# Kernel tuning notes

Measured on AMD Instinct MI355X. Metric: run time of the kernel, lower is better.

## Reference

```python
import jax, jax.numpy as jnp
import numpy as np

D_MODEL = 1024
N_HEADS = 4
KEY_DIM = 1024   # expand_k=1.0
VALUE_DIM = 2048 # expand_v=2.0
DK = KEY_DIM // N_HEADS    # 256
DV = VALUE_DIM // N_HEADS  # 512
LOW_RANK = 16
GATE_NORM = 16.0
EPS = 1e-5


def setup_inputs() -> dict:
    key = jax.random.key(0)
    ks = jax.random.split(key, 10)
    B, L = 2, 2048
    gain = 2.0 ** (-2.5)

    def xavier(k, shape, g=gain):
        fan_in, fan_out = shape[0], shape[1]
        a = g * np.sqrt(6.0 / (fan_in + fan_out))
        return jax.random.uniform(k, shape, jnp.float32, -a, a)

    return {
        "x": jax.random.normal(ks[0], (B, L, D_MODEL), jnp.float32),
        "Wq": xavier(ks[1], (D_MODEL, KEY_DIM)),
        "Wk": xavier(ks[2], (D_MODEL, KEY_DIM)),
        "Wv": xavier(ks[3], (D_MODEL, VALUE_DIM)),
        "Wg": xavier(ks[4], (D_MODEL, VALUE_DIM)),
        "gk_w1": xavier(ks[5], (D_MODEL, LOW_RANK)),
        "gk_w2": xavier(ks[6], (LOW_RANK, KEY_DIM)),
        "gk_b2": jnp.zeros((KEY_DIM,), jnp.float32),
        "g_norm_w": jnp.ones((DV,), jnp.float32),
        "Wo": xavier(ks[7], (VALUE_DIM, D_MODEL)),
    }


def _gla_scan(q, k, v, gk):
    # q,k: [B,H,L,Dk]; v: [B,H,L,Dv]; gk: [B,H,L,Dk] (log decay)
    # recurrence: S_t = diag(exp(gk_t)) S_{t-1} + k_t v_t^T ; o_t = q_t S_t
    B, H, L, dk = q.shape
    dv = v.shape[-1]
    # time-major for scan
    qs = jnp.moveaxis(q, 2, 0)
    ks_ = jnp.moveaxis(k, 2, 0)
    vs = jnp.moveaxis(v, 2, 0)
    gs = jnp.moveaxis(gk, 2, 0)

    def step(S, inp):
        q_t, k_t, v_t, g_t = inp  # [B,H,Dk], [B,H,Dk], [B,H,Dv], [B,H,Dk]
        S = S * jnp.exp(g_t)[..., None] + k_t[..., None] * v_t[..., None, :]
        o_t = jnp.einsum('bhk,bhkv->bhv', q_t, S)
        return S, o_t

    S0 = jnp.zeros((B, H, dk, dv), q.dtype)
    _, os = jax.lax.scan(step, S0, (qs, ks_, vs, gs))
    return jnp.moveaxis(os, 0, 2)  # [B,H,L,Dv]


def reference(x, Wq, Wk, Wv, Wg, gk_w1, gk_w2, gk_b2, g_norm_w, Wo):
    B, L, _ = x.shape
    scale = DK ** -0.5

    def heads(t, d):
        return t.reshape(B, L, N_HEADS, d).transpose(0, 2, 1, 3)  # b h l d

    q = heads(x @ Wq, DK) * scale
    k = heads(x @ Wk, DK)
    v = heads(x @ Wv, DV)
    gk = heads(jax.nn.log_sigmoid((x @ gk_w1) @ gk_w2 + gk_b2) / GATE_NORM, DK)

    o = _gla_scan(q, k, v, gk)                 # [B,H,L,Dv]
    o = o.transpose(0, 2, 1, 3)                # [B,L,H,Dv]

    g = (x @ Wg).reshape(B, L, N_HEADS, DV)
    # FusedRMSNormSwishGate: RMSNorm(o) * silu(g)
    rms = o * jax.lax.rsqrt(jnp.mean(o * o, axis=-1, keepdims=True) + EPS)
    o = (rms * g_norm_w) * (g * jax.nn.sigmoid(g))
    o = o.reshape(B, L, VALUE_DIM)
    return o @ Wo
```

## Files before the change

kernel.cpp:

```cpp
#include <hip/hip_runtime.h>
#include <hip/hip_bf16.h>
#include <math.h>

#define NHEADS 4
#define DKH 256
#define DVH 512
#define SEQL 2048
#define NB 2
#define NTOK (NB*SEQL)
#define DM 1024
#define KDT 1024
#define VDT 2048
#define CHUNK 128
#define NCH (SEQL/CHUNK)

typedef unsigned short u16;
typedef unsigned int   u32;
typedef unsigned long long u64;
typedef __attribute__((ext_vector_type(8))) short bf16x8;
typedef __attribute__((ext_vector_type(4))) float f32x4;

__device__ inline u16 f2bf(float f) {
  __hip_bfloat16 h = __float2bfloat16(f);
  return *reinterpret_cast<u16*>(&h);
}
__device__ inline float bf2f(u16 u) {
  u32 x = ((u32)u) << 16;
  return __uint_as_float(x);
}

__device__ __forceinline__ void gload16(const u16* g, u16* l) {
  __builtin_amdgcn_global_load_lds(
      (const __attribute__((address_space(1))) u32*)g,
      (__attribute__((address_space(3))) u32*)l,
      16, 0, 0);
}

__global__ __launch_bounds__(256)
void f2bf_kernel(const float* __restrict__ in, u16* __restrict__ out, int n)
{
  const int i = (blockIdx.x * 256 + threadIdx.x) * 8;
  if (i >= n) return;
  const float4 x0 = *(const float4*)&in[i];
  const float4 x1 = *(const float4*)&in[i + 4];
  int4 p;
  p.x = f2bf(x0.x) | ((u32)f2bf(x0.y) << 16);
  p.y = f2bf(x0.z) | ((u32)f2bf(x0.w) << 16);
  p.z = f2bf(x1.x) | ((u32)f2bf(x1.y) << 16);
  p.w = f2bf(x1.z) | ((u32)f2bf(x1.w) << 16);
  *(int4*)&out[i] = p;
}

__global__ __launch_bounds__(256)
void transpose_f2bf(const float* __restrict__ W, u16* __restrict__ Wt, int K, int N)
{
  __shared__ float Ts[64][69];
  const int n0 = blockIdx.x * 64, k0 = blockIdx.y * 64;
  const int tx = threadIdx.x & 15, ty = threadIdx.x >> 4;
  #pragma unroll
  for (int r = 0; r < 4; ++r) {
    const int k = ty + r * 16;
    const float4 w4 = *(const float4*)&W[(size_t)(k0 + k) * N + n0 + tx * 4];
    Ts[tx*4 + 0][k] = w4.x;
    Ts[tx*4 + 1][k] = w4.y;
    Ts[tx*4 + 2][k] = w4.z;
    Ts[tx*4 + 3][k] = w4.w;
  }
  __syncthreads();
  #pragma unroll
  for (int r = 0; r < 4; ++r) {
    const int n = ty + r * 16;
    u64 pk = (u64)f2bf(Ts[n][tx*4 + 0]) | ((u64)f2bf(Ts[n][tx*4 + 1]) << 16)
           | ((u64)f2bf(Ts[n][tx*4 + 2]) << 32) | ((u64)f2bf(Ts[n][tx*4 + 3]) << 48);
    *(u64*)&Wt[(size_t)(n0 + n) * K + k0 + tx * 4] = pk;
  }
}

__global__ __launch_bounds__(256)
void gemm_qkvg(const u16* __restrict__ A, const u16* __restrict__ Wall,
               float* __restrict__ Qb, float* __restrict__ Kbf,
               u16* __restrict__ Vt, float* __restrict__ Gb, float qscale)
{
  __shared__ __align__(16) u16 As[128 * 32];
  __shared__ __align__(16) u16 Bs[128 * 32];
  const int tid = threadIdx.x;
  const int lane = tid & 63, wave = tid >> 6;
  const int wr = wave >> 1, wc = wave & 1;
  const int l15 = lane & 15, l4 = lane >> 4;
  const int bx = blockIdx.x;
  const int bm = blockIdx.y * 128, bn = bx * 128;

  f32x4 acc[4][4];
  #pragma unroll
  for (int i = 0; i < 4; ++i)
    #pragma unroll
    for (int j = 0; j < 4; ++j)
      acc[i][j] = (f32x4){0.f, 0.f, 0.f, 0.f};

  const int sRow = wave * 32 + (lane >> 2);
  const int sCol = (lane & 3) * 8;
  const u16* Ag0 = &A   [(size_t)(bm + sRow) * DM + sCol];
  const u16* Ag1 = &A   [(size_t)(bm + sRow + 16) * DM + sCol];
  const u16* Bg0 = &Wall[(size_t)(bn + sRow) * DM + sCol];
  const u16* Bg1 = &Wall[(size_t)(bn + sRow + 16) * DM + sCol];
  u16* Al0 = &As[(wave * 32) * 32];
  u16* Al1 = &As[(wave * 32 + 16) * 32];
  u16* Bl0 = &Bs[(wave * 32) * 32];
  u16* Bl1 = &Bs[(wave * 32 + 16) * 32];

  for (int k0 = 0; k0 < DM; k0 += 32) {
    gload16(Ag0 + k0, Al0);
    gload16(Ag1 + k0, Al1);
    gload16(Bg0 + k0, Bl0);
    gload16(Bg1 + k0, Bl1);
    __syncthreads();
    bf16x8 af[4], bfv[4];
    #pragma unroll
    for (int mi = 0; mi < 4; ++mi)
      af[mi] = *(const bf16x8*)&As[(wr*64 + mi*16 + l15) * 32 + l4*8];
    #pragma unroll
    for (int ni = 0; ni < 4; ++ni)
      bfv[ni] = *(const bf16x8*)&Bs[(wc*64 + ni*16 + l15) * 32 + l4*8];
    #pragma unroll
    for (int mi = 0; mi < 4; ++mi)
      #pragma unroll
      for (int ni = 0; ni < 4; ++ni)
        acc[mi][ni] = __builtin_amdgcn_mfma_f32_16x16x32_bf16(af[mi], bfv[ni], acc[mi][ni], 0, 0, 0);
    __syncthreads();
  }

  if (bx < 8) {
    #pragma unroll
    for (int mi = 0; mi < 4; ++mi)
      #pragma unroll
      for (int ni = 0; ni < 4; ++ni) {
        const int col = bn + wc*64 + ni*16 + l15;
        #pragma unroll
        for (int r = 0; r < 4; ++r)
          Qb[(size_t)(bm + wr*64 + mi*16 + l4*4 + r) * 1024 + col] = acc[mi][ni][r] * qscale;
      }
  } else if (bx < 16) {
    #pragma unroll
    for (int mi = 0; mi < 4; ++mi)
      #pragma unroll
      for (int ni = 0; ni < 4; ++ni) {
        const int col = bn - 1024 + wc*64 + ni*16 + l15;
        #pragma unroll
        for (int r = 0; r < 4; ++r)
          Kbf[(size_t)(bm + wr*64 + mi*16 + l4*4 + r) * 1024 + col] = acc[mi][ni][r];
      }
  } else if (bx < 32) {
    #pragma unroll
    for (int mi = 0; mi < 4; ++mi) {
      const int row0 = bm + wr*64 + mi*16 + l4*4;
      const int b = row0 >> 11, l = row0 & 2047;
      #pragma unroll
      for (int ni = 0; ni < 4; ++ni) {
        const int colV = bn - 2048 + wc*64 + ni*16 + l15;
        const int h = colV >> 9, dv = colV & 511;
        u64 pk = (u64)f2bf(acc[mi][ni][0]) | ((u64)f2bf(acc[mi][ni][1]) << 16)
               | ((u64)f2bf(acc[mi][ni][2]) << 32) | ((u64)f2bf(acc[mi][ni][3]) << 48);
        *(u64*)&Vt[((size_t)((b*4 + h)*512 + dv)) * SEQL + l] = pk;
      }
    }
  } else {
    #pragma unroll
    for (int mi = 0; mi < 4; ++mi)
      #pragma unroll
      for (int ni = 0; ni < 4; ++ni) {
        const int col = bn - 4096 + wc*64 + ni*16 + l15;
        #pragma unroll
        for (int r = 0; r < 4; ++r)
          Gb[(size_t)(bm + wr*64 + mi*16 + l4*4 + r) * 2048 + col] = acc[mi][ni][r];
      }
  }
}

__global__ __launch_bounds__(256)
void gemm_bf16(const u16* __restrict__ A, const u16* __restrict__ Bt,
               float* __restrict__ C, int M, int N, int K, float scale)
{
  __shared__ __align__(16) u16 As[128 * 40];
  __shared__ __align__(16) u16 Bs[128 * 40];
  const int tid = threadIdx.x;
  const int lane = tid & 63, wave = tid >> 6;
  const int wr = wave >> 1, wc = wave & 1;
  const int l15 = lane & 15, l4 = lane >> 4;
  const int bm = blockIdx.y * 128, bn = blockIdx.x * 128;

  f32x4 acc[4][4];
  #pragma unroll
  for (int i = 0; i < 4; ++i)
    #pragma unroll
    for (int j = 0; j < 4; ++j)
      acc[i][j] = (f32x4){0.f, 0.f, 0.f, 0.f};

  const int srow = tid >> 2;
  const int scol = (tid & 3) * 8;
  const u16* Ag = &A [(size_t)(bm + srow) * K + scol];
  const u16* Bg = &Bt[(size_t)(bn + srow) * K + scol];

  int4 a0 = *(const int4*)(Ag);
  int4 a1 = *(const int4*)(Ag + (size_t)64 * K);
  int4 b0 = *(const int4*)(Bg);
  int4 b1 = *(const int4*)(Bg + (size_t)64 * K);

  for (int k0 = 0; k0 < K; k0 += 32) {
    __syncthreads();
    *(int4*)&As[(srow)      * 40 + scol] = a0;
    *(int4*)&As[(64 + srow) * 40 + scol] = a1;
    *(int4*)&Bs[(srow)      * 40 + scol] = b0;
    *(int4*)&Bs[(64 + srow) * 40 + scol] = b1;
    __syncthreads();
    if (k0 + 32 < K) {
      a0 = *(const int4*)(Ag + k0 + 32);
      a1 = *(const int4*)(Ag + (size_t)64 * K + k0 + 32);
      b0 = *(const int4*)(Bg + k0 + 32);
      b1 = *(const int4*)(Bg + (size_t)64 * K + k0 + 32);
    }
    bf16x8 af[4], bfv[4];
    #pragma unroll
    for (int mi = 0; mi < 4; ++mi)
      af[mi] = *(const bf16x8*)&As[(wr*64 + mi*16 + l15) * 40 + l4*8];
    #pragma unroll
    for (int ni = 0; ni < 4; ++ni)
      bfv[ni] = *(const bf16x8*)&Bs[(wc*64 + ni*16 + l15) * 40 + l4*8];
    #pragma unroll
    for (int mi = 0; mi < 4; ++mi)
      #pragma unroll
      for (int ni = 0; ni < 4; ++ni)
        acc[mi][ni] = __builtin_amdgcn_mfma_f32_16x16x32_bf16(af[mi], bfv[ni], acc[mi][ni], 0, 0, 0);
  }

  #pragma unroll
  for (int mi = 0; mi < 4; ++mi)
    #pragma unroll
    for (int ni = 0; ni < 4; ++ni) {
      const int col = bn + wc*64 + ni*16 + l15;
      #pragma unroll
      for (int r = 0; r < 4; ++r) {
        const int row = bm + wr*64 + mi*16 + l4*4 + r;
        C[(size_t)row * N + col] = acc[mi][ni][r] * scale;
      }
    }
}

__global__ __launch_bounds__(256)
void gemm_u(const float* __restrict__ X, const float* __restrict__ W1,
            float* __restrict__ U)
{
  __shared__ float Xs[64][65];
  __shared__ __align__(16) float W1s[64][16];
  const int tid = threadIdx.x;
  const int row0 = blockIdx.x * 64;
  const int rr = tid & 63, gg = tid >> 6;
  float acc[4] = {0.f, 0.f, 0.f, 0.f};
  for (int k0 = 0; k0 < DM; k0 += 64) {
    #pragma unroll
    for (int rep = 0; rep < 4; ++rep) {
      const int m = (tid >> 4) + rep * 16;
      const int kk = (tid & 15) << 2;
      const float4 x4 = *(const float4*)&X[(size_t)(row0 + m) * DM + k0 + kk];
      Xs[kk+0][m] = x4.x; Xs[kk+1][m] = x4.y; Xs[kk+2][m] = x4.z; Xs[kk+3][m] = x4.w;
    }
    {
      const int kk = tid >> 2, n = (tid & 3) << 2;
      *(float4*)&W1s[kk][n] = *(const float4*)&W1[(size_t)(k0 + kk) * 16 + n];
    }
    __syncthreads();
    #pragma unroll
    for (int k2 = 0; k2 < 64; ++k2) {
      const float xv = Xs[k2][rr];
      const float4 w4 = *(const float4*)&W1s[k2][gg << 2];
      acc[0] += xv * w4.x; acc[1] += xv * w4.y; acc[2] += xv * w4.z; acc[3] += xv * w4.w;
    }
    __syncthreads();
  }
  *(float4*)&U[(size_t)(row0 + rr) * 16 + (gg << 2)] =
      make_float4(acc[0], acc[1], acc[2], acc[3]);
}

__device__ inline float ls_exp(float z) {
  const float ls = (z >= 0.f) ? -log1pf(expf(-z)) : (z - log1pf(expf(z)));
  return expf(ls * 0.0625f);
}

__global__ __launch_bounds__(256)
void gate_kernel(const float* __restrict__ U, const float* __restrict__ W2,
                 const float* __restrict__ b2, float* __restrict__ EGKo)
{
  __shared__ float Us[16];
  const int row = blockIdx.x, tid = threadIdx.x;
  if (tid < 16) Us[tid] = U[row * 16 + tid];
  __syncthreads();
  const int d0 = tid << 2;
  float4 z = *(const float4*)&b2[d0];
  #pragma unroll
  for (int r = 0; r < 16; ++r) {
    const float u = Us[r];
    const float4 w4 = *(const float4*)&W2[r * 1024 + d0];
    z.x += u * w4.x; z.y += u * w4.y; z.z += u * w4.z; z.w += u * w4.w;
  }
  float4 e = make_float4(ls_exp(z.x), ls_exp(z.y), ls_exp(z.z), ls_exp(z.w));
  *(float4*)&EGKo[(size_t)row * 1024 + d0] = e;
}

__global__ __launch_bounds__(256)
void chunk_prep(const float* __restrict__ Q, const float* __restrict__ K,
                const float* __restrict__ EG, u16* __restrict__ qtb,
                u16* __restrict__ ktb, u16* __restrict__ khb,
                float* __restrict__ lamC)
{
  const int j = blockIdx.x;
  const int bh = blockIdx.y;
  const int b = bh >> 2, h = bh & 3;
  const int tid = threadIdx.x;
  const size_t base = ((size_t)(b * SEQL + j * CHUNK)) * KDT + h * DKH + tid;
  float cum = 1.f;
  for (int t = 0; t < CHUNK; t += 4) {
    const size_t i0 = base + (size_t)t * KDT;
    float d[4], q[4], k[4];
    #pragma unroll
    for (int u = 0; u < 4; ++u) {
      d[u] = EG[i0 + (size_t)u * KDT];
      q[u] = Q [i0 + (size_t)u * KDT];
      k[u] = K [i0 + (size_t)u * KDT];
    }
    #pragma unroll
    for (int u = 0; u < 4; ++u) {
      cum *= d[u];
      qtb[i0 + (size_t)u * KDT] = f2bf(q[u] * cum);
      ktb[i0 + (size_t)u * KDT] = f2bf(k[u] / cum);
    }
  }
  lamC[(bh * NCH + j) * 256 + tid] = cum;
  for (int t = 0; t < CHUNK; t += 4) {
    const size_t i0 = base + (size_t)t * KDT;
    u16 kt4[4];
    #pragma unroll
    for (int u = 0; u < 4; ++u) kt4[u] = ktb[i0 + (size_t)u * KDT];
    #pragma unroll
    for (int u = 0; u < 4; ++u)
      khb[i0 + (size_t)u * KDT] = f2bf(bf2f(kt4[u]) * cum);
  }
}

__global__ __launch_bounds__(256)
void gla_pstate_mfma(const u16* __restrict__ kh, const u16* __restrict__ Vt,
                     float* __restrict__ P)
{
  const int mb = blockIdx.x, nb = blockIdx.y, jc = blockIdx.z;
  const int bh = jc >> 4, j = jc & 15;
  const int b = bh >> 2, h = bh & 3;
  const int tid = threadIdx.x;
  const int lane = tid & 63, wave = tid >> 6;
  const int wr = wave >> 1, wc = wave & 1;
  const int l15 = lane & 15, l4 = lane >> 4;
  const int tok0 = b * SEQL + j * CHUNK;

  __shared__ __align__(16) u16 Al[128 * 40];
  __shared__ __align__(16) u16 Blt[128 * 40];

  f32x4 acc[4][4];
  #pragma unroll
  for (int i = 0; i < 4; ++i)
    #pragma unroll
    for (int jj = 0; jj < 4; ++jj) acc[i][jj] = (f32x4){0.f,0.f,0.f,0.f};

  for (int kt0 = 0; kt0 < CHUNK; kt0 += 32) {
    {
      const int srow = tid >> 2, scol = (tid & 3) * 8;
      *(int4*)&Al[(srow)    * 40 + scol] =
        *(const int4*)&Vt[((size_t)(bh*512 + mb*128 + srow))    * SEQL + j*CHUNK + kt0 + scol];
      *(int4*)&Al[(64+srow) * 40 + scol] =
        *(const int4*)&Vt[((size_t)(bh*512 + mb*128 + 64+srow)) * SEQL + j*CHUNK + kt0 + scol];
    }
    {
      const int t = tid & 31;
      #pragma unroll
      for (int i = 0; i < 2; ++i) {
        const int dkg = (tid >> 5) * 16 + i * 8;
        int4 v = *(const int4*)&kh[(size_t)(tok0 + kt0 + t) * KDT + h*DKH + nb*128 + dkg];
        const u16* pv = (const u16*)&v;
        #pragma unroll
        for (int u = 0; u < 8; ++u) Blt[(dkg + u)*40 + t] = pv[u];
      }
    }
    __syncthreads();
    bf16x8 af[4], bv[4];
    #pragma unroll
    for (int mi = 0; mi < 4; ++mi)
      af[mi] = *(const bf16x8*)&Al[(wr*64 + mi*16 + l15)*40 + l4*8];
    #pragma unroll
    for (int ni = 0; ni < 4; ++ni)
      bv[ni] = *(const bf16x8*)&Blt[(wc*64 + ni*16 + l15)*40 + l4*8];
    #pragma unroll
    for (int mi = 0; mi < 4; ++mi)
      #pragma unroll
      for (int ni = 0; ni < 4; ++ni)
        acc[mi][ni] = __builtin_amdgcn_mfma_f32_16x16x32_bf16(af[mi], bv[ni], acc[mi][ni], 0, 0, 0);
    __syncthreads();
  }

  #pragma unroll
  for (int mi = 0; mi < 4; ++mi)
    #pragma unroll
    for (int ni = 0; ni < 4; ++ni) {
      const int col = nb*128 + wc*64 + ni*16 + l15;
      #pragma unroll
      for (int r = 0; r < 4; ++r) {
        const int row = mb*128 + wr*64 + mi*16 + l4*4 + r;
        P[(size_t)jc * 131072 + (size_t)row * 256 + col] = acc[mi][ni][r];
      }
    }
}

__global__ __launch_bounds__(256)
void gla_sscan(const float* __restrict__ P, const float* __restrict__ lamC,
               u16* __restrict__ SjT)
{
  const int bh = blockIdx.y;
  const int e0 = blockIdx.x * 1024 + threadIdx.x * 4;
  const int dv = e0 >> 8, dk = e0 & 255;
  float4 S = make_float4(0.f, 0.f, 0.f, 0.f);
  for (int j = 0; j < NCH; ++j) {
    const size_t cb = (size_t)(bh * NCH + j);
    const float4 lam = *(const float4*)&lamC[cb * 256 + dk];
    const size_t idx = cb * 131072 + (size_t)dv * 256 + dk;
    const float4 tmp = *(const float4*)&P[idx];
    u64 pk = (u64)f2bf(S.x) | ((u64)f2bf(S.y) << 16)
           | ((u64)f2bf(S.z) << 32) | ((u64)f2bf(S.w) << 48);
    *(u64*)&SjT[idx] = pk;
    S.x = lam.x * S.x + tmp.x;
    S.y = lam.y * S.y + tmp.y;
    S.z = lam.z * S.z + tmp.z;
    S.w = lam.w * S.w + tmp.w;
  }
}

__global__ __launch_bounds__(256)
void gla_intra_mfma(const u16* __restrict__ qt, const u16* __restrict__ kt,
                    const u16* __restrict__ Vt, const u16* __restrict__ SjT,
                    float* __restrict__ O)
{
  const int half = blockIdx.x;
  const int j    = blockIdx.y;
  const int bh   = blockIdx.z;
  const int b = bh >> 2, h = bh & 3;
  const int tid = threadIdx.x;
  const int lane = tid & 63, wave = tid >> 6;
  const int wr = wave >> 1, wc = wave & 1;
  const int l15 = lane & 15, l4 = lane >> 4;
  const int tok0 = b * SEQL + j * CHUNK;

  __shared__ __align__(16) u16 Pl[128 * 136];
  __shared__ __align__(16) u16 stg[128 * 136];
  u16* As = stg;
  u16* Bs = stg + 128 * 40;

  const size_t qkBase = (size_t)tok0 * KDT + h * DKH;
  const size_t sjBase = (size_t)(bh * NCH + j) * 131072;

  const int srow = tid >> 2;
  const int scol = (tid & 3) * 8;

  f32x4 acc[4][4];
  #pragma unroll
  for (int i = 0; i < 4; ++i)
    #pragma unroll
    for (int jj = 0; jj < 4; ++jj) acc[i][jj] = (f32x4){0.f,0.f,0.f,0.f};

  int4 ra0 = *(const int4*)&qt[qkBase + (size_t)srow      * KDT + scol];
  int4 ra1 = *(const int4*)&qt[qkBase + (size_t)(64+srow) * KDT + scol];
  int4 rb0 = *(const int4*)&kt[qkBase + (size_t)srow      * KDT + scol];
  int4 rb1 = *(const int4*)&kt[qkBase + (size_t)(64+srow) * KDT + scol];

  for (int dk0 = 0; dk0 < DKH; dk0 += 32) {
    __syncthreads();
    *(int4*)&As[(srow)    * 40 + scol] = ra0;
    *(int4*)&As[(64+srow) * 40 + scol] = ra1;
    *(int4*)&Bs[(srow)    * 40 + scol] = rb0;
    *(int4*)&Bs[(64+srow) * 40 + scol] = rb1;
    __syncthreads();
    if (dk0 + 32 < DKH) {
      ra0 = *(const int4*)&qt[qkBase + (size_t)srow      * KDT + dk0 + 32 + scol];
      ra1 = *(const int4*)&qt[qkBase + (size_t)(64+srow) * KDT + dk0 + 32 + scol];
      rb0 = *(const int4*)&kt[qkBase + (size_t)srow      * KDT + dk0 + 32 + scol];
      rb1 = *(const int4*)&kt[qkBase + (size_t)(64+srow) * KDT + dk0 + 32 + scol];
    }
    bf16x8 af[4], bv[4];
    #pragma unroll
    for (int mi = 0; mi < 4; ++mi)
      af[mi] = *(const bf16x8*)&As[(wr*64 + mi*16 + l15) * 40 + l4*8];
    #pragma unroll
    for (int ni = 0; ni < 4; ++ni)
      bv[ni] = *(const bf16x8*)&Bs[(wc*64 + ni*16 + l15) * 40 + l4*8];
    #pragma unroll
    for (int mi = 0; mi < 4; ++mi)
      #pragma unroll
      for (int ni = 0; ni < 4; ++ni)
        acc[mi][ni] = __builtin_amdgcn_mfma_f32_16x16x32_bf16(af[mi], bv[ni], acc[mi][ni], 0, 0, 0);
  }
  __syncthreads();

  #pragma unroll
  for (int mi = 0; mi < 4; ++mi)
    #pragma unroll
    for (int ni = 0; ni < 4; ++ni) {
      const int s = wc*64 + ni*16 + l15;
      #pragma unroll
      for (int r = 0; r < 4; ++r) {
        const int t = wr*64 + mi*16 + l4*4 + r;
        Pl[t*136 + s] = (s <= t) ? f2bf(acc[mi][ni][r]) : (u16)0;
      }
    }
  __syncthreads();

  for (int dt = 0; dt < 2; ++dt) {
    const int dvBase = half*256 + dt*128;
    f32x4 acc2[4][4];
    #pragma unroll
    for (int i = 0; i < 4; ++i)
      #pragma unroll
      for (int jj = 0; jj < 4; ++jj) acc2[i][jj] = (f32x4){0.f,0.f,0.f,0.f};

    int4 ia0 = *(const int4*)&qt [qkBase + (size_t)srow      * KDT + scol];
    int4 ia1 = *(const int4*)&qt [qkBase + (size_t)(64+srow) * KDT + scol];
    int4 ib0 = *(const int4*)&SjT[sjBase + (size_t)(dvBase + srow)      * 256 + scol];
    int4 ib1 = *(const int4*)&SjT[sjBase + (size_t)(dvBase + 64 + srow) * 256 + scol];

    for (int k0 = 0; k0 < DKH; k0 += 32) {
      __syncthreads();
      *(int4*)&As[(srow)    * 40 + scol] = ia0;
      *(int4*)&As[(64+srow) * 40 + scol] = ia1;
      *(int4*)&Bs[(srow)    * 40 + scol] = ib0;
      *(int4*)&Bs[(64+srow) * 40 + scol] = ib1;
      __syncthreads();
      if (k0 + 32 < DKH) {
        ia0 = *(const int4*)&qt [qkBase + (size_t)srow      * KDT + k0 + 32 + scol];
        ia1 = *(const int4*)&qt [qkBase + (size_t)(64+srow) * KDT + k0 + 32 + scol];
        ib0 = *(const int4*)&SjT[sjBase + (size_t)(dvBase + srow)      * 256 + k0 + 32 + scol];
        ib1 = *(const int4*)&SjT[sjBase + (size_t)(dvBase + 64 + srow) * 256 + k0 + 32 + scol];
      }
      bf16x8 af[4], bv[4];
      #pragma unroll
      for (int mi = 0; mi < 4; ++mi)
        af[mi] = *(const bf16x8*)&As[(wr*64 + mi*16 + l15) * 40 + l4*8];
      #pragma unroll
      for (int ni = 0; ni < 4; ++ni)
        bv[ni] = *(const bf16x8*)&Bs[(wc*64 + ni*16 + l15) * 40 + l4*8];
      #pragma unroll
      for (int mi = 0; mi < 4; ++mi)
        #pragma unroll
        for (int ni = 0; ni < 4; ++ni)
          acc2[mi][ni] = __builtin_amdgcn_mfma_f32_16x16x32_bf16(af[mi], bv[ni], acc2[mi][ni], 0, 0, 0);
    }
    __syncthreads();

    #pragma unroll
    for (int i = 0; i < 8; ++i) {
      const int row = i*16 + (tid >> 4);
      const int col8 = (tid & 15) * 8;
      *(int4*)&stg[row*136 + col8] =
        *(const int4*)&Vt[((size_t)(bh*512 + dvBase + row)) * SEQL + j*CHUNK + col8];
    }
    __syncthreads();
    #pragma unroll
    for (int ks = 0; ks < 4; ++ks) {
      bf16x8 af2[4], bv2[4];
      #pragma unroll
      for (int mi = 0; mi < 4; ++mi)
        af2[mi] = *(const bf16x8*)&Pl[(wr*64 + mi*16 + l15)*136 + ks*32 + l4*8];
      #pragma unroll
      for (int ni = 0; ni < 4; ++ni)
        bv2[ni] = *(const bf16x8*)&stg[(wc*64 + ni*16 + l15)*136 + ks*32 + l4*8];
      #pragma unroll
      for (int mi = 0; mi < 4; ++mi)
        #pragma unroll
        for (int ni = 0; ni < 4; ++ni)
          acc2[mi][ni] = __builtin_amdgcn_mfma_f32_16x16x32_bf16(af2[mi], bv2[ni], acc2[mi][ni], 0, 0, 0);
    }
    #pragma unroll
    for (int mi = 0; mi < 4; ++mi)
      #pragma unroll
      for (int ni = 0; ni < 4; ++ni) {
        const int col = h*DVH + dvBase + wc*64 + ni*16 + l15;
        #pragma unroll
        for (int r = 0; r < 4; ++r) {
          const int row = tok0 + wr*64 + mi*16 + l4*4 + r;
          O[(size_t)row * VDT + col] = acc2[mi][ni][r];
        }
      }
    __syncthreads();
  }
}

__global__ __launch_bounds__(256)
void epilogue(const float* __restrict__ O, const float* __restrict__ G,
              const float* __restrict__ w, u16* __restrict__ Y)
{
  const int row = blockIdx.x;
  const int tid = threadIdx.x;
  __shared__ float sred[4];
  for (int h = 0; h < NHEADS; ++h) {
    const size_t base = (size_t)row * VDT + h * DVH;
    const float2 o2 = *(const float2*)&O[base + tid * 2];
    float ss = o2.x * o2.x + o2.y * o2.y;
    #pragma unroll
    for (int off = 32; off > 0; off >>= 1) ss += __shfl_down(ss, off);
    if ((tid & 63) == 0) sred[tid >> 6] = ss;
    __syncthreads();
    const float tot = sred[0] + sred[1] + sred[2] + sred[3];
    const float rs = rsqrtf(tot * (1.f / DVH) + 1e-5f);
    const float2 g2 = *(const float2*)&G[base + tid * 2];
    const float2 w2 = *(const float2*)&w[tid * 2];
    const float y0 = o2.x * rs * w2.x * g2.x / (1.f + expf(-g2.x));
    const float y1 = o2.y * rs * w2.y * g2.y / (1.f + expf(-g2.y));
    const u32 pk = (u32)f2bf(y0) | ((u32)f2bf(y1) << 16);
    *(u32*)&Y[base + tid * 2] = pk;
    __syncthreads();
  }
}

extern "C" void kernel_launch(void* const* d_in, const int* in_sizes, int n_in,
                              void* d_out, int out_size, void* d_ws, size_t ws_size,
                              hipStream_t stream)
{
  const float* x    = (const float*)d_in[0];
  const float* Wq   = (const float*)d_in[1];
  const float* Wk   = (const float*)d_in[2];
  const float* Wv   = (const float*)d_in[3];
  const float* Wg   = (const float*)d_in[4];
  const float* gw1  = (const float*)d_in[5];
  const float* gw2  = (const float*)d_in[6];
  const float* gb2  = (const float*)d_in[7];
  const float* gnw  = (const float*)d_in[8];
  const float* Wo   = (const float*)d_in[9];
  float* out = (float*)d_out;

  float* ws = (float*)d_ws;
  const size_t M = 1024ull * 1024ull;
  float* Qb   = ws;
  float* Kbf  = ws + 4*M;
  float* EGK  = ws + 8*M;
  u16*   Vtb  = (u16*)(ws + 12*M);
  u16*   qtb  = (u16*)(ws + 16*M);
  u16*   ktb  = (u16*)(ws + 18*M);
  float* Gb   = ws + 20*M;
  float* Ob   = ws + 28*M;
  float* Sjb  = ws + 36*M;
  float* lamC = ws + 52*M;
  float* Ub   = ws + 52*M + 32768;
  u16*   khb  = (u16*)(ws + 53*M);
  u16*   Wallb= (u16*)(ws + 55*M);
  u16*   xb   = (u16*)(ws + 58*M);
  u16*   SjTb = (u16*)(ws + 53*M);
  u16*   Wob  = (u16*)Kbf;
  u16*   Y2b  = (u16*)Qb;

  const float qscale = 0.0625f;

  f2bf_kernel  <<<2048, 256, 0, stream>>>(x, xb, NTOK * DM);
  transpose_f2bf<<<dim3(16, 16), 256, 0, stream>>>(Wq, Wallb,                1024, 1024);
  transpose_f2bf<<<dim3(16, 16), 256, 0, stream>>>(Wk, Wallb + 1024*1024,    1024, 1024);
  transpose_f2bf<<<dim3(32, 16), 256, 0, stream>>>(Wv, Wallb + 2048*1024,    1024, 2048);
  transpose_f2bf<<<dim3(32, 16), 256, 0, stream>>>(Wg, Wallb + 4096ull*1024, 1024, 2048);

  gemm_qkvg<<<dim3(48, 32), 256, 0, stream>>>(xb, Wallb, Qb, Kbf, Vtb, Gb, qscale);
  gemm_u      <<<64, 256, 0, stream>>>(x, gw1, Ub);
  gate_kernel <<<NTOK, 256, 0, stream>>>(Ub, gw2, gb2, EGK);

  chunk_prep<<<dim3(NCH, 8), 256, 0, stream>>>(Qb, Kbf, EGK, qtb, ktb, khb, lamC);

  transpose_f2bf<<<dim3(16, 32), 256, 0, stream>>>(Wo, Wob, 2048, 1024);

  gla_pstate_mfma<<<dim3(4, 2, 128), 256, 0, stream>>>(khb, Vtb, Sjb);
  gla_sscan      <<<dim3(128, 8), 256, 0, stream>>>(Sjb, lamC, SjTb);
  gla_intra_mfma <<<dim3(2, NCH, 8), 256, 0, stream>>>(qtb, ktb, Vtb, SjTb, Ob);

  epilogue<<<NTOK, 256, 0, stream>>>(Ob, Gb, gnw, Y2b);
  gemm_bf16<<<dim3(8, 32), 256, 0, stream>>>(Y2b, Wob, out, NTOK, 1024, 2048, 1.f);
}
```

Baseline: 312.6 us.

## Double-buffer LDS in GEMMs and store Q/K/G intermediates as bf16

Both MFMA GEMMs now use two LDS buffers, issuing the direct global-to-LDS load for the next K-slice before computing on the current one, with a single barrier per iteration. The gemm_bf16 kernel swaps its register-staged loads for the same gload16 path as gemm_qkvg. Q, K and G projections are written as bf16 instead of fp32, halving their write and read traffic in chunk_prep and the epilogue. The workspace layout is rearranged to fit; the cost is bf16 rounding of Q/K/G before the scan and gate, and doubled LDS per block.

```diff
diff --git a/kernel.cpp b/kernel.cpp
--- a/kernel.cpp
+++ b/kernel.cpp
@@ -78,11 +78,11 @@
 
 __global__ __launch_bounds__(256)
 void gemm_qkvg(const u16* __restrict__ A, const u16* __restrict__ Wall,
-               float* __restrict__ Qb, float* __restrict__ Kbf,
-               u16* __restrict__ Vt, float* __restrict__ Gb, float qscale)
-{
-  __shared__ __align__(16) u16 As[128 * 32];
-  __shared__ __align__(16) u16 Bs[128 * 32];
+               u16* __restrict__ Qh, u16* __restrict__ Kh,
+               u16* __restrict__ Vt, u16* __restrict__ Gh, float qscale)
+{
+  __shared__ __align__(16) u16 As[2][128 * 32];
+  __shared__ __align__(16) u16 Bs[2][128 * 32];
   const int tid = threadIdx.x;
   const int lane = tid & 63, wave = tid >> 6;
   const int wr = wave >> 1, wc = wave & 1;
@@ -103,24 +103,29 @@
   const u16* Ag1 = &A   [(size_t)(bm + sRow + 16) * DM + sCol];
   const u16* Bg0 = &Wall[(size_t)(bn + sRow) * DM + sCol];
   const u16* Bg1 = &Wall[(size_t)(bn + sRow + 16) * DM + sCol];
-  u16* Al0 = &As[(wave * 32) * 32];
-  u16* Al1 = &As[(wave * 32 + 16) * 32];
-  u16* Bl0 = &Bs[(wave * 32) * 32];
-  u16* Bl1 = &Bs[(wave * 32 + 16) * 32];
+  const int lb0 = (wave * 32) * 32, lb1 = (wave * 32 + 16) * 32;
+
+  gload16(Ag0, &As[0][lb0]);
+  gload16(Ag1, &As[0][lb1]);
+  gload16(Bg0, &Bs[0][lb0]);
+  gload16(Bg1, &Bs[0][lb1]);
+  __syncthreads();
 
   for (int k0 = 0; k0 < DM; k0 += 32) {
-    gload16(Ag0 + k0, Al0);
-    gload16(Ag1 + k0, Al1);
-    gload16(Bg0 + k0, Bl0);
-    gload16(Bg1 + k0, Bl1);
-    __syncthreads();
+    const int cur = (k0 >> 5) & 1;
+    if (k0 + 32 < DM) {
+      gload16(Ag0 + k0 + 32, &As[cur ^ 1][lb0]);
+      gload16(Ag1 + k0 + 32, &As[cur ^ 1][lb1]);
+      gload16(Bg0 + k0 + 32, &Bs[cur ^ 1][lb0]);
+      gload16(Bg1 + k0 + 32, &Bs[cur ^ 1][lb1]);
+    }
     bf16x8 af[4], bfv[4];
     #pragma unroll
     for (int mi = 0; mi < 4; ++mi)
-      af[mi] = *(const bf16x8*)&As[(wr*64 + mi*16 + l15) * 32 + l4*8];
+      af[mi] = *(const bf16x8*)&As[cur][(wr*64 + mi*16 + l15) * 32 + l4*8];
     #pragma unroll
     for (int ni = 0; ni < 4; ++ni)
-      bfv[ni] = *(const bf16x8*)&Bs[(wc*64 + ni*16 + l15) * 32 + l4*8];
+      bfv[ni] = *(const bf16x8*)&Bs[cur][(wc*64 + ni*16 + l15) * 32 + l4*8];
     #pragma unroll
     for (int mi = 0; mi < 4; ++mi)
       #pragma unroll
@@ -137,7 +142,7 @@
         const int col = bn + wc*64 + ni*16 + l15;
         #pragma unroll
         for (int r = 0; r < 4; ++r)
-          Qb[(size_t)(bm + wr*64 + mi*16 + l4*4 + r) * 1024 + col] = acc[mi][ni][r] * qscale;
+          Qh[(size_t)(bm + wr*64 + mi*16 + l4*4 + r) * 1024 + col] = f2bf(acc[mi][ni][r] * qscale);
       }
   } else if (bx < 16) {
     #pragma unroll
@@ -147,7 +152,7 @@
         const int col = bn - 1024 + wc*64 + ni*16 + l15;
         #pragma unroll
         for (int r = 0; r < 4; ++r)
-          Kbf[(size_t)(bm + wr*64 + mi*16 + l4*4 + r) * 1024 + col] = acc[mi][ni][r];
+          Kh[(size_t)(bm + wr*64 + mi*16 + l4*4 + r) * 1024 + col] = f2bf(acc[mi][ni][r]);
       }
   } else if (bx < 32) {
     #pragma unroll
@@ -171,7 +176,7 @@
         const int col = bn - 4096 + wc*64 + ni*16 + l15;
         #pragma unroll
         for (int r = 0; r < 4; ++r)
-          Gb[(size_t)(bm + wr*64 + mi*16 + l4*4 + r) * 2048 + col] = acc[mi][ni][r];
+          Gh[(size_t)(bm + wr*64 + mi*16 + l4*4 + r) * 2048 + col] = f2bf(acc[mi][ni][r]);
       }
   }
 }
@@ -180,8 +185,8 @@
 void gemm_bf16(const u16* __restrict__ A, const u16* __restrict__ Bt,
                float* __restrict__ C, int M, int N, int K, float scale)
 {
-  __shared__ __align__(16) u16 As[128 * 40];
-  __shared__ __align__(16) u16 Bs[128 * 40];
+  __shared__ __align__(16) u16 As[2][128 * 32];
+  __shared__ __align__(16) u16 Bs[2][128 * 32];
   const int tid = threadIdx.x;
   const int lane = tid & 63, wave = tid >> 6;
   const int wr = wave >> 1, wc = wave & 1;
@@ -195,41 +200,41 @@
     for (int j = 0; j < 4; ++j)
       acc[i][j] = (f32x4){0.f, 0.f, 0.f, 0.f};
 
-  const int srow = tid >> 2;
-  const int scol = (tid & 3) * 8;
-  const u16* Ag = &A [(size_t)(bm + srow) * K + scol];
-  const u16* Bg = &Bt[(size_t)(bn + srow) * K + scol];
-
-  int4 a0 = *(const int4*)(Ag);
-  int4 a1 = *(const int4*)(Ag + (size_t)64 * K);
-  int4 b0 = *(const int4*)(Bg);
-  int4 b1 = *(const int4*)(Bg + (size_t)64 * K);
+  const int sRow = wave * 32 + (lane >> 2);
+  const int sCol = (lane & 3) * 8;
+  const u16* Ag0 = &A [(size_t)(bm + sRow) * K + sCol];
+  const u16* Ag1 = &A [(size_t)(bm + sRow + 16) * K + sCol];
+  const u16* Bg0 = &Bt[(size_t)(bn + sRow) * K + sCol];
+  const u16* Bg1 = &Bt[(size_t)(bn + sRow + 16) * K + sCol];
+  const int lb0 = (wave * 32) * 32, lb1 = (wave * 32 + 16) * 32;
+
+  gload16(Ag0, &As[0][lb0]);
+  gload16(Ag1, &As[0][lb1]);
+  gload16(Bg0, &Bs[0][lb0]);
+  gload16(Bg1, &Bs[0][lb1]);
+  __syncthreads();
 
   for (int k0 = 0; k0 < K; k0 += 32) {
-    __syncthreads();
-    *(int4*)&As[(srow)      * 40 + scol] = a0;
-    *(int4*)&As[(64 + srow) * 40 + scol] = a1;
-    *(int4*)&Bs[(srow)      * 40 + scol] = b0;
-    *(int4*)&Bs[(64 + srow) * 40 + scol] = b1;
-    __syncthreads();
+    const int cur = (k0 >> 5) & 1;
     if (k0 + 32 < K) {
-      a0 = *(const int4*)(Ag + k0 + 32);
-      a1 = *(const int4*)(Ag + (size_t)64 * K + k0 + 32);
-      b0 = *(const int4*)(Bg + k0 + 32);
-      b1 = *(const int4*)(Bg + (size_t)64 * K + k0 + 32);
+      gload16(Ag0 + k0 + 32, &As[cur ^ 1][lb0]);
+      gload16(Ag1 + k0 + 32, &As[cur ^ 1][lb1]);
+      gload16(Bg0 + k0 + 32, &Bs[cur ^ 1][lb0]);
+      gload16(Bg1 + k0 + 32, &Bs[cur ^ 1][lb1]);
     }
     bf16x8 af[4], bfv[4];
     #pragma unroll
     for (int mi = 0; mi < 4; ++mi)
-      af[mi] = *(const bf16x8*)&As[(wr*64 + mi*16 + l15) * 40 + l4*8];
+      af[mi] = *(const bf16x8*)&As[cur][(wr*64 + mi*16 + l15) * 32 + l4*8];
     #pragma unroll
     for (int ni = 0; ni < 4; ++ni)
-      bfv[ni] = *(const bf16x8*)&Bs[(wc*64 + ni*16 + l15) * 40 + l4*8];
+      bfv[ni] = *(const bf16x8*)&Bs[cur][(wc*64 + ni*16 + l15) * 32 + l4*8];
     #pragma unroll
     for (int mi = 0; mi < 4; ++mi)
       #pragma unroll
       for (int ni = 0; ni < 4; ++ni)
         acc[mi][ni] = __builtin_amdgcn_mfma_f32_16x16x32_bf16(af[mi], bfv[ni], acc[mi][ni], 0, 0, 0);
+    __syncthreads();
   }
 
   #pragma unroll
@@ -306,7 +311,7 @@
 }
 
 __global__ __launch_bounds__(256)
-void chunk_prep(const float* __restrict__ Q, const float* __restrict__ K,
+void chunk_prep(const u16* __restrict__ Qh, const u16* __restrict__ Kh,
                 const float* __restrict__ EG, u16* __restrict__ qtb,
                 u16* __restrict__ ktb, u16* __restrict__ khb,
                 float* __restrict__ lamC)
@@ -323,8 +328,8 @@
     #pragma unroll
     for (int u = 0; u < 4; ++u) {
       d[u] = EG[i0 + (size_t)u * KDT];
-      q[u] = Q [i0 + (size_t)u * KDT];
-      k[u] = K [i0 + (size_t)u * KDT];
+      q[u] = bf2f(Qh[i0 + (size_t)u * KDT]);
+      k[u] = bf2f(Kh[i0 + (size_t)u * KDT]);
     }
     #pragma unroll
     for (int u = 0; u < 4; ++u) {
@@ -596,7 +601,7 @@
 }
 
 __global__ __launch_bounds__(256)
-void epilogue(const float* __restrict__ O, const float* __restrict__ G,
+void epilogue(const float* __restrict__ O, const u16* __restrict__ G,
               const float* __restrict__ w, u16* __restrict__ Y)
 {
   const int row = blockIdx.x;
@@ -612,10 +617,12 @@
     __syncthreads();
     const float tot = sred[0] + sred[1] + sred[2] + sred[3];
     const float rs = rsqrtf(tot * (1.f / DVH) + 1e-5f);
-    const float2 g2 = *(const float2*)&G[base + tid * 2];
+    const u32 g2p = *(const u32*)&G[base + tid * 2];
+    const float gx = bf2f((u16)(g2p & 0xffff));
+    const float gy = bf2f((u16)(g2p >> 16));
     const float2 w2 = *(const float2*)&w[tid * 2];
-    const float y0 = o2.x * rs * w2.x * g2.x / (1.f + expf(-g2.x));
-    const float y1 = o2.y * rs * w2.y * g2.y / (1.f + expf(-g2.y));
+    const float y0 = o2.x * rs * w2.x * gx / (1.f + expf(-gx));
+    const float y1 = o2.y * rs * w2.y * gy / (1.f + expf(-gy));
     const u32 pk = (u32)f2bf(y0) | ((u32)f2bf(y1) << 16);
     *(u32*)&Y[base + tid * 2] = pk;
     __syncthreads();
@@ -640,23 +647,23 @@
 
   float* ws = (float*)d_ws;
   const size_t M = 1024ull * 1024ull;
-  float* Qb   = ws;
-  float* Kbf  = ws + 4*M;
-  float* EGK  = ws + 8*M;
-  u16*   Vtb  = (u16*)(ws + 12*M);
-  u16*   qtb  = (u16*)(ws + 16*M);
-  u16*   ktb  = (u16*)(ws + 18*M);
-  float* Gb   = ws + 20*M;
-  float* Ob   = ws + 28*M;
-  float* Sjb  = ws + 36*M;
-  float* lamC = ws + 52*M;
-  float* Ub   = ws + 52*M + 32768;
-  u16*   khb  = (u16*)(ws + 53*M);
-  u16*   Wallb= (u16*)(ws + 55*M);
-  u16*   xb   = (u16*)(ws + 58*M);
+  u16*   Qbh  = (u16*)(ws);
+  u16*   Kbh  = (u16*)(ws + 2*M);
+  float* EGK  = ws + 4*M;
+  u16*   Vtb  = (u16*)(ws + 8*M);
+  u16*   qtb  = (u16*)(ws + 12*M);
+  u16*   ktb  = (u16*)(ws + 14*M);
+  u16*   Gbh  = (u16*)(ws + 16*M);
+  float* Ob   = ws + 20*M;
+  float* Sjb  = ws + 28*M;
+  float* lamC = ws + 44*M;
+  float* Ub   = ws + 44*M + 32768;
+  u16*   khb  = (u16*)(ws + 45*M);
+  u16*   xb   = (u16*)(ws + 47*M);
+  u16*   Wallb= (u16*)(ws + 49*M);
+  u16*   Wob  = (u16*)(ws + 52*M);
   u16*   SjTb = (u16*)(ws + 53*M);
-  u16*   Wob  = (u16*)Kbf;
-  u16*   Y2b  = (u16*)Qb;
+  u16*   Y2b  = (u16*)(ws);
 
   const float qscale = 0.0625f;
 
@@ -665,19 +672,18 @@
   transpose_f2bf<<<dim3(16, 16), 256, 0, stream>>>(Wk, Wallb + 1024*1024,    1024, 1024);
   transpose_f2bf<<<dim3(32, 16), 256, 0, stream>>>(Wv, Wallb + 2048*1024,    1024, 2048);
   transpose_f2bf<<<dim3(32, 16), 256, 0, stream>>>(Wg, Wallb + 4096ull*1024, 1024, 2048);
-
-  gemm_qkvg<<<dim3(48, 32), 256, 0, stream>>>(xb, Wallb, Qb, Kbf, Vtb, Gb, qscale);
+  transpose_f2bf<<<dim3(16, 32), 256, 0, stream>>>(Wo, Wob, 2048, 1024);
+
+  gemm_qkvg<<<dim3(48, 32), 256, 0, stream>>>(xb, Wallb, Qbh, Kbh, Vtb, Gbh, qscale);
   gemm_u      <<<64, 256, 0, stream>>>(x, gw1, Ub);
   gate_kernel <<<NTOK, 256, 0, stream>>>(Ub, gw2, gb2, EGK);
 
-  chunk_prep<<<dim3(NCH, 8), 256, 0, stream>>>(Qb, Kbf, EGK, qtb, ktb, khb, lamC);
-
-  transpose_f2bf<<<dim3(16, 32), 256, 0, stream>>>(Wo, Wob, 2048, 1024);
+  chunk_prep<<<dim3(NCH, 8), 256, 0, stream>>>(Qbh, Kbh, EGK, qtb, ktb, khb, lamC);
 
   gla_pstate_mfma<<<dim3(4, 2, 128), 256, 0, stream>>>(khb, Vtb, Sjb);
   gla_sscan      <<<dim3(128, 8), 256, 0, stream>>>(Sjb, lamC, SjTb);
   gla_intra_mfma <<<dim3(2, NCH, 8), 256, 0, stream>>>(qtb, ktb, Vtb, SjTb, Ob);
 
-  epilogue<<<NTOK, 256, 0, stream>>>(Ob, Gb, gnw, Y2b);
+  epilogue<<<NTOK, 256, 0, stream>>>(Ob, Gbh, gnw, Y2b);
   gemm_bf16<<<dim3(8, 32), 256, 0, stream>>>(Y2b, Wob, out, NTOK, 1024, 2048, 1.f);
 }
```

Measured after the change: 301.3 us. 1.04x faster.
